# Optimization experiments

Measured on AMD Instinct MI355X. Metric: run time of the kernel, lower is better.

Reference implementation:

```python
import jax, jax.numpy as jnp
import numpy as np

E = 1024
H = 16
D = E // H  # head_dim = 64
B, L, S = 2, 2048, 2048


def setup_inputs() -> dict:
    key = jax.random.key(0)
    ks = jax.random.split(key, 10)
    scale = 1.0 / np.sqrt(E)
    return {
        "x": jax.random.normal(ks[0], (B, L, E), jnp.float32),
        "context": jax.random.normal(ks[1], (B, S, E), jnp.float32),
        "Wq": jax.random.normal(ks[2], (E, E), jnp.float32) * scale,
        "bq": jnp.zeros((E,), jnp.float32),
        "Wk": jax.random.normal(ks[3], (E, E), jnp.float32) * scale,
        "bk": jnp.zeros((E,), jnp.float32),
        "Wv": jax.random.normal(ks[4], (E, E), jnp.float32) * scale,
        "bv": jnp.zeros((E,), jnp.float32),
        "Wp": jax.random.normal(ks[5], (E, E), jnp.float32) * scale,
        "bp": jnp.zeros((E,), jnp.float32),
    }


def reference(x, context, Wq, bq, Wk, bk, Wv, bv, Wp, bp):
    b, l, _ = x.shape
    s = context.shape[1]
    # linear projections then split heads: [B, H, L/S, D]
    q = (x @ Wq + bq).reshape(b, l, H, D).transpose(0, 2, 1, 3)
    k = (context @ Wk + bk).reshape(b, s, H, D).transpose(0, 2, 1, 3)
    v = (context @ Wv + bv).reshape(b, s, H, D).transpose(0, 2, 1, 3)
    # scores [B, H, L, S]
    attn = jnp.einsum("bhld,bhsd->bhls", q, k) / jnp.sqrt(jnp.float32(D))
    attn = jax.nn.softmax(attn, axis=-1)
    # dropout is identity in eval mode
    out = jnp.einsum("bhls,bhsd->bhld", attn, v)
    out = out.transpose(0, 2, 1, 3).reshape(b, l, E)
    return out @ Wp + bp
```

## Files before the change

### kernel.cpp

```cpp
#include <hip/hip_runtime.h>
#include <math.h>

#define B_ 2
#define L_ 2048
#define S_ 2048
#define E_ 1024
#define H_ 16
#define D_ 64
#define SC_ 0.180336880111120f

typedef unsigned short u16;
typedef unsigned int u32;
typedef __attribute__((ext_vector_type(8))) short short8;
typedef __attribute__((ext_vector_type(4))) float floatx4;

__device__ __forceinline__ u16 f2bf(float f) {
    union { float f; unsigned u; } a; a.f = f;
    unsigned r = a.u + 0x7FFFu + ((a.u >> 16) & 1u);
    return (u16)(r >> 16);
}

__device__ __forceinline__ u32 cvt_pk_bf16(float lo, float hi) {
    u32 d;
    asm("v_cvt_pk_bf16_f32 %0, %1, %2" : "=v"(d) : "v"(lo), "v"(hi));
    return d;
}

__device__ __forceinline__ void pl32swap(u32& a, u32& b) {
    asm("v_permlane32_swap_b32 %0, %1" : "+v"(a), "+v"(b));
}
__device__ __forceinline__ void pl16swap(u32& a, u32& b) {
    asm("v_permlane16_swap_b32 %0, %1" : "+v"(a), "+v"(b));
}

__device__ __forceinline__ void glds16(const u16* g, u16* l) {
    __builtin_amdgcn_global_load_lds(
        (const __attribute__((address_space(1))) void*)g,
        (__attribute__((address_space(3))) void*)l, 16, 0, 0);
}

__global__ void prep_kernel(const float* __restrict__ x, const float* __restrict__ ctx,
                            u16* __restrict__ Xb, u16* __restrict__ Cb,
                            const float* __restrict__ Wq, const float* __restrict__ Wk,
                            const float* __restrict__ Wv, const float* __restrict__ Wp,
                            u16* __restrict__ WqT, u16* __restrict__ WkT,
                            u16* __restrict__ WvT, u16* __restrict__ WpT) {
    __shared__ float tile[32][33];
    const int bid = blockIdx.x;
    const int tid = threadIdx.x;
    if (bid < 4096) {
        const int sub = bid;
        const float* src = sub < 2048 ? x : ctx;
        u16* dst = sub < 2048 ? Xb : Cb;
        int i = (sub & 2047) * 256 + tid;
        float4 u0 = ((const float4*)src)[2 * i];
        float4 u1 = ((const float4*)src)[2 * i + 1];
        uint4 o;
        o.x = cvt_pk_bf16(u0.x, u0.y);
        o.y = cvt_pk_bf16(u0.z, u0.w);
        o.z = cvt_pk_bf16(u1.x, u1.y);
        o.w = cvt_pk_bf16(u1.z, u1.w);
        ((uint4*)dst)[i] = o;
    } else {
        const int t = bid - 4096;
        const int z = t >> 10;
        const int rem = t & 1023;
        const float* W = z == 0 ? Wq : (z == 1 ? Wk : (z == 2 ? Wv : Wp));
        u16* Wt = z == 0 ? WqT : (z == 1 ? WkT : (z == 2 ? WvT : WpT));
        const int bx = (rem & 31) * 32, by = (rem >> 5) * 32;
        const int tx = tid & 31, ty = tid >> 5;
#pragma unroll
        for (int j = 0; j < 4; ++j)
            tile[ty + j * 8][tx] = W[(size_t)(by + ty + j * 8) * E_ + bx + tx];
        __syncthreads();
#pragma unroll
        for (int j = 0; j < 4; ++j)
            Wt[(size_t)(bx + ty + j * 8) * E_ + by + tx] = f2bf(tile[tx][ty + j * 8]);
    }
}

__device__ __forceinline__ void xcd_remap64(int bx, int by, int& m_idx, int& n_idx) {
    int lin = bx + 8 * by;
    int c8 = lin & 7;
    int g = lin >> 3;
    m_idx = c8 + 8 * (g & 7);
    n_idx = g >> 3;
}

__global__ __launch_bounds__(256, 3) void qkv_gemm_kernel(
    const u16* __restrict__ Xb, const u16* __restrict__ Cb,
    const u16* __restrict__ WqT, const u16* __restrict__ WkT, const u16* __restrict__ WvT,
    const float* __restrict__ bq, const float* __restrict__ bk, const float* __restrict__ bv,
    u16* __restrict__ Qb, u16* __restrict__ Kb, u16* __restrict__ Vtb) {
    __shared__ __align__(16) u16 sm[24576];

    const int z = blockIdx.z;
    const u16* A  = z == 0 ? Xb : Cb;
    const u16* Bt = z == 0 ? WqT : (z == 1 ? WkT : WvT);
    const float* bias = z == 0 ? bq : (z == 1 ? bk : bv);
    const float scale = z == 0 ? SC_ : 1.0f;

    const int tid = threadIdx.x;
    const int lane = tid & 63;
    const int wv = tid >> 6;
    const int wm = wv >> 1, wn = wv & 1;
    const int qd = lane >> 4, lr = lane & 15;
    int m_idx, n_idx;
    xcd_remap64(blockIdx.x, blockIdx.y, m_idx, n_idx);
    const int m0 = m_idx * 64, n0 = n_idx * 128;
    const int lrow = lane >> 3;
    const int gu = (lane & 7) ^ lrow;

    floatx4 acc[2][4];
#pragma unroll
    for (int i = 0; i < 2; ++i)
#pragma unroll
        for (int j = 0; j < 4; ++j) {
            floatx4 zz = {0.f, 0.f, 0.f, 0.f};
            acc[i][j] = zz;
        }

#define STAGE_AB(buf, kb)                                                          \
    {                                                                              \
        _Pragma("unroll") for (int j = 0; j < 2; ++j) {                            \
            int c = wv * 2 + j;                                                    \
            glds16(A + (size_t)(m0 + c * 8 + lrow) * E_ + (kb) + gu * 8,           \
                   sm + (buf)*4096 + c * 512);                                     \
        }                                                                          \
        _Pragma("unroll") for (int j = 0; j < 4; ++j) {                            \
            int c = wv * 4 + j;                                                    \
            glds16(Bt + (size_t)(n0 + c * 8 + lrow) * E_ + (kb) + gu * 8,          \
                   sm + 8192 + (buf)*8192 + c * 512);                              \
        }                                                                          \
    }

    STAGE_AB(0, 0)
    __syncthreads();

    for (int t = 0; t < 16; ++t) {
        const int cur = t & 1;
        if (t + 1 < 16) STAGE_AB(cur ^ 1, (t + 1) * 64)

        short8 af[2][2], bf[4][2];
#pragma unroll
        for (int mi = 0; mi < 2; ++mi)
#pragma unroll
            for (int kk = 0; kk < 2; ++kk) {
                int row = wm * 32 + mi * 16 + lr;
                int u = (kk * 4 + qd) ^ (lr & 7);
                af[mi][kk] = *(const short8*)(sm + cur * 4096 + row * 64 + u * 8);
            }
#pragma unroll
        for (int ni = 0; ni < 4; ++ni)
#pragma unroll
            for (int kk = 0; kk < 2; ++kk) {
                int row = wn * 64 + ni * 16 + lr;
                int u = (kk * 4 + qd) ^ (lr & 7);
                bf[ni][kk] = *(const short8*)(sm + 8192 + cur * 8192 + row * 64 + u * 8);
            }
        __builtin_amdgcn_s_setprio(1);
#pragma unroll
        for (int kk = 0; kk < 2; ++kk)
#pragma unroll
            for (int mi = 0; mi < 2; ++mi)
#pragma unroll
                for (int ni = 0; ni < 4; ++ni)
                    acc[mi][ni] = __builtin_amdgcn_mfma_f32_16x16x32_bf16(
                        af[mi][kk], bf[ni][kk], acc[mi][ni], 0, 0, 0);
        __builtin_amdgcn_s_setprio(0);

        __syncthreads();
    }

    if (z == 2) {
        const int CTS = 72;
#pragma unroll
        for (int mi = 0; mi < 2; ++mi)
#pragma unroll
            for (int ni = 0; ni < 4; ++ni) {
                int col = wn * 64 + ni * 16 + lr;
                int row = wm * 32 + mi * 16 + qd * 4;
                float bv_ = bias[n0 + col];
                u16 h0 = f2bf(acc[mi][ni][0] + bv_);
                u16 h1 = f2bf(acc[mi][ni][1] + bv_);
                u16 h2 = f2bf(acc[mi][ni][2] + bv_);
                u16 h3 = f2bf(acc[mi][ni][3] + bv_);
                uint2 pk;
                pk.x = h0 | ((u32)h1 << 16);
                pk.y = h2 | ((u32)h3 << 16);
                *(uint2*)&sm[col * CTS + row] = pk;
            }
        __syncthreads();
        const int d = tid >> 1;
        const int sh = (tid & 1) * 32;
        const int bidx = m0 >> 11;
        const int sloc = m0 & (S_ - 1);
        u16* dstV = Vtb + ((size_t)(bidx * E_ + n0 + d)) * S_ + sloc + sh;
        const u16* srcC = sm + d * CTS + sh;
#pragma unroll
        for (int j = 0; j < 4; ++j)
            *(uint4*)(dstV + j * 8) = *(const uint4*)(srcC + j * 8);
    } else {
        u16* Cq = z == 0 ? Qb : Kb;
#pragma unroll
        for (int mi = 0; mi < 2; ++mi) {
#pragma unroll
            for (int ni = 0; ni < 4; ++ni) {
                int col = n0 + wn * 64 + ni * 16 + lr;
                float bv_ = bias[col];
#pragma unroll
                for (int r = 0; r < 4; ++r) {
                    int row = m0 + wm * 32 + mi * 16 + qd * 4 + r;
                    Cq[(size_t)row * E_ + col] = f2bf((acc[mi][ni][r] + bv_) * scale);
                }
            }
        }
    }
#undef STAGE_AB
}

__global__ __launch_bounds__(256, 4) void flash_attn_kernel(
    const u16* __restrict__ Q, const u16* __restrict__ Kg,
    const u16* __restrict__ Vtg, u16* __restrict__ Opart, float* __restrict__ lpart) {
    __shared__ __align__(16) u16 Ks[2][64 * 64];
    __shared__ __align__(16) u16 Vs[2][64 * 64];

    const int tid = threadIdx.x;
    const int lane = tid & 63;
    const int wv = tid >> 6;
    const int qd = lane >> 4, lr = lane & 15;

    const int lin = blockIdx.x + 16 * (blockIdx.y + 32 * blockIdx.z);
    const int c8 = lin & 7;
    const int slot = lin >> 3;
    const int qx = slot & 15;
    const int grp = c8 + 8 * (slot >> 4);
    const int bh = grp & 31;
    const int z = grp >> 5;
    const int b = bh >> 4, h = bh & 15;
    const int q0 = qx * 128;
    const int sbeg = z * (S_ / 2);

    u16* Op = Opart + (size_t)z * (B_ * L_ * E_);
    float* lp = lpart + (size_t)z * (B_ * H_ * L_);

    const u16* Kbase = Kg + (size_t)(b * S_) * E_ + h * D_;
    const u16* Vbase = Vtg + (size_t)(b * E_ + h * D_) * S_;

    const int lrow = lane >> 3;
    const int gu = (lane & 7) ^ lrow;

#pragma unroll
    for (int j = 0; j < 2; ++j) {
        int c = wv * 2 + j;
        glds16(Kbase + (size_t)(sbeg + c * 8 + lrow) * E_ + gu * 8, &Ks[0][c * 512]);
        glds16(Vbase + (size_t)(c * 8 + lrow) * S_ + sbeg + gu * 8, &Vs[0][c * 512]);
    }

    short8 qf[2][2];
#pragma unroll
    for (int mi = 0; mi < 2; ++mi)
#pragma unroll
        for (int kk = 0; kk < 2; ++kk)
            qf[mi][kk] = *(const short8*)(Q + (size_t)(b * L_ + q0 + wv * 32 + mi * 16 + lr) * E_ +
                                          h * D_ + kk * 32 + qd * 8);

    const short one_bf = (short)0x3F80;
    short8 ones8 = {one_bf, one_bf, one_bf, one_bf, one_bf, one_bf, one_bf, one_bf};

    floatx4 o_acc[2][4];
    floatx4 l4[2];
#pragma unroll
    for (int mi = 0; mi < 2; ++mi) {
#pragma unroll
        for (int nt = 0; nt < 4; ++nt) {
            floatx4 z4 = {0.f, 0.f, 0.f, 0.f};
            o_acc[mi][nt] = z4;
        }
        floatx4 z4 = {0.f, 0.f, 0.f, 0.f};
        l4[mi] = z4;
    }

    __syncthreads();

    const int NIT = (S_ / 2) / 64;

    for (int it = 0; it < NIT; ++it) {
        const int cur = it & 1;
        if (it + 1 < NIT) {
            int s1 = sbeg + (it + 1) * 64;
#pragma unroll
            for (int j = 0; j < 2; ++j) {
                int c = wv * 2 + j;
                glds16(Kbase + (size_t)(s1 + c * 8 + lrow) * E_ + gu * 8, &Ks[cur ^ 1][c * 512]);
                glds16(Vbase + (size_t)(c * 8 + lrow) * S_ + s1 + gu * 8, &Vs[cur ^ 1][c * 512]);
            }
        }

        floatx4 s_[2][4];
        __builtin_amdgcn_s_setprio(1);
#pragma unroll
        for (int nt = 0; nt < 4; ++nt) {
            int krow = nt * 16 + lr;
            short8 kb0 = *(const short8*)(&Ks[cur][krow * 64 + ((qd) ^ (lr & 7)) * 8]);
            short8 kb1 = *(const short8*)(&Ks[cur][krow * 64 + ((4 + qd) ^ (lr & 7)) * 8]);
#pragma unroll
            for (int mi = 0; mi < 2; ++mi) {
                floatx4 zz = {0.f, 0.f, 0.f, 0.f};
                zz = __builtin_amdgcn_mfma_f32_16x16x32_bf16(kb0, qf[mi][0], zz, 0, 0, 0);
                zz = __builtin_amdgcn_mfma_f32_16x16x32_bf16(kb1, qf[mi][1], zz, 0, 0, 0);
                s_[mi][nt] = zz;
            }
        }
        __builtin_amdgcn_s_setprio(0);

        short8 pf[2][2];
#pragma unroll
        for (int mi = 0; mi < 2; ++mi) {
            u32 dg[4][2];
#pragma unroll
            for (int nt = 0; nt < 4; ++nt) {
                float p0 = __builtin_amdgcn_exp2f(s_[mi][nt][0]);
                float p1 = __builtin_amdgcn_exp2f(s_[mi][nt][1]);
                float p2 = __builtin_amdgcn_exp2f(s_[mi][nt][2]);
                float p3 = __builtin_amdgcn_exp2f(s_[mi][nt][3]);
                dg[nt][0] = cvt_pk_bf16(p0, p1);
                dg[nt][1] = cvt_pk_bf16(p2, p3);
            }
#pragma unroll
            for (int kk = 0; kk < 2; ++kk) {
                u32 x0 = dg[2 * kk][0], y0 = dg[2 * kk + 1][0];
                pl32swap(x0, y0);
                pl16swap(x0, y0);
                u32 x1 = dg[2 * kk][1], y1 = dg[2 * kk + 1][1];
                pl32swap(x1, y1);
                pl16swap(x1, y1);
                union { u32 d[4]; short8 v; } u;
                u.d[0] = x0; u.d[1] = x1; u.d[2] = y0; u.d[3] = y1;
                pf[mi][kk] = u.v;
            }
        }

        __builtin_amdgcn_s_setprio(1);
#pragma unroll
        for (int mi = 0; mi < 2; ++mi) {
            l4[mi] = __builtin_amdgcn_mfma_f32_16x16x32_bf16(pf[mi][0], ones8, l4[mi], 0, 0, 0);
            l4[mi] = __builtin_amdgcn_mfma_f32_16x16x32_bf16(pf[mi][1], ones8, l4[mi], 0, 0, 0);
        }
#pragma unroll
        for (int nt = 0; nt < 4; ++nt) {
            int vrow = nt * 16 + lr;
            short8 vb0 = *(const short8*)(&Vs[cur][vrow * 64 + ((qd) ^ (lr & 7)) * 8]);
            short8 vb1 = *(const short8*)(&Vs[cur][vrow * 64 + ((4 + qd) ^ (lr & 7)) * 8]);
#pragma unroll
            for (int mi = 0; mi < 2; ++mi) {
                o_acc[mi][nt] = __builtin_amdgcn_mfma_f32_16x16x32_bf16(pf[mi][0], vb0, o_acc[mi][nt], 0, 0, 0);
                o_acc[mi][nt] = __builtin_amdgcn_mfma_f32_16x16x32_bf16(pf[mi][1], vb1, o_acc[mi][nt], 0, 0, 0);
            }
        }
        __builtin_amdgcn_s_setprio(0);

        __syncthreads();
    }

    float linv[2][4];
#pragma unroll
    for (int mi = 0; mi < 2; ++mi) {
        if (lr == 0) {
#pragma unroll
            for (int r = 0; r < 4; ++r)
                lp[(size_t)(b * H_ + h) * L_ + q0 + wv * 32 + mi * 16 + qd * 4 + r] = l4[mi][r];
        }
#pragma unroll
        for (int r = 0; r < 4; ++r) linv[mi][r] = 1.0f / l4[mi][r];
    }

#pragma unroll
    for (int mi = 0; mi < 2; ++mi)
#pragma unroll
        for (int nt = 0; nt < 4; ++nt)
#pragma unroll
            for (int r = 0; r < 4; ++r) {
                int row = q0 + wv * 32 + mi * 16 + qd * 4 + r;
                int col = h * D_ + nt * 16 + lr;
                Op[(size_t)(b * L_ + row) * E_ + col] = f2bf(o_acc[mi][nt][r] * linv[mi][r]);
            }
}

__global__ __launch_bounds__(256, 2) void out_gemm_kernel(
    const u16* __restrict__ O1, const u16* __restrict__ O2,
    const float* __restrict__ l1, const float* __restrict__ l2,
    const u16* __restrict__ WpT, const float* __restrict__ bp,
    float* __restrict__ out) {
    __shared__ __align__(16) u16 As[2][64 * 64];
    __shared__ __align__(16) u16 Bs[2][128 * 64];

    const int tid = threadIdx.x;
    const int lane = tid & 63;
    const int wv = tid >> 6;
    const int wm = wv >> 1, wn = wv & 1;
    const int qd = lane >> 4, lr = lane & 15;

    int m_idx, n_idx;
    xcd_remap64(blockIdx.x, blockIdx.y, m_idx, n_idx);
    const int m0 = m_idx * 64, n0 = n_idx * 128;
    const int lrow = lane >> 3;
    const int gu = (lane & 7) ^ lrow;

    floatx4 acc[2][4];
#pragma unroll
    for (int i = 0; i < 2; ++i)
#pragma unroll
        for (int j = 0; j < 4; ++j) {
            floatx4 zz = {0.f, 0.f, 0.f, 0.f};
            acc[i][j] = zz;
        }

    uint4 p1[2], p2[2];
    float la_[2], lb_[2];

#define LOAD_AO(tt)                                                                \
    {                                                                              \
        _Pragma("unroll") for (int j = 0; j < 2; ++j) {                            \
            int c = wv * 2 + j;                                                    \
            int row = m0 + c * 8 + lrow;                                           \
            int col = (tt)*64 + gu * 8;                                            \
            p1[j] = *(const uint4*)(O1 + (size_t)row * E_ + col);                  \
            p2[j] = *(const uint4*)(O2 + (size_t)row * E_ + col);                  \
            int li = (row >> 11) * (H_ * L_) + (tt)*L_ + (row & (L_ - 1));         \
            la_[j] = l1[li];                                                       \
            lb_[j] = l2[li];                                                       \
        }                                                                          \
    }

#define WRITE_AO(buf)                                                              \
    {                                                                              \
        _Pragma("unroll") for (int j = 0; j < 2; ++j) {                            \
            int c = wv * 2 + j;                                                    \
            float s = 1.0f / (la_[j] + lb_[j]);                                    \
            float w1 = la_[j] * s, w2 = lb_[j] * s;                                \
            const u32* pa = (const u32*)&p1[j];                                    \
            const u32* pb = (const u32*)&p2[j];                                    \
            uint4 o;                                                               \
            u32* po = (u32*)&o;                                                    \
            _Pragma("unroll") for (int d = 0; d < 4; ++d) {                        \
                union { u32 u; float f; } x0, x1, y0, y1;                          \
                x0.u = pa[d] << 16; x1.u = pa[d] & 0xFFFF0000u;                    \
                y0.u = pb[d] << 16; y1.u = pb[d] & 0xFFFF0000u;                    \
                po[d] = cvt_pk_bf16(x0.f * w1 + y0.f * w2, x1.f * w1 + y1.f * w2); \
            }                                                                      \
            *(uint4*)(&As[buf][c * 512 + lane * 8]) = o;                           \
        }                                                                          \
    }

#define STAGE_BO(buf, kb)                                                          \
    {                                                                              \
        _Pragma("unroll") for (int j = 0; j < 4; ++j) {                            \
            int c = wv * 4 + j;                                                    \
            glds16(WpT + (size_t)(n0 + c * 8 + lrow) * E_ + (kb) + gu * 8,         \
                   &Bs[buf][c * 512]);                                             \
        }                                                                          \
    }

    LOAD_AO(0)
    STAGE_BO(0, 0)
    WRITE_AO(0)
    __syncthreads();

    for (int t = 0; t < 16; ++t) {
        const int cur = t & 1;
        if (t + 1 < 16) {
            STAGE_BO(cur ^ 1, (t + 1) * 64)
            LOAD_AO(t + 1)
        }

        short8 af[2][2], bf[4][2];
#pragma unroll
        for (int mi = 0; mi < 2; ++mi)
#pragma unroll
            for (int kk = 0; kk < 2; ++kk) {
                int row = wm * 32 + mi * 16 + lr;
                int u = (kk * 4 + qd) ^ (lr & 7);
                af[mi][kk] = *(const short8*)(&As[cur][row * 64 + u * 8]);
            }
#pragma unroll
        for (int ni = 0; ni < 4; ++ni)
#pragma unroll
            for (int kk = 0; kk < 2; ++kk) {
                int row = wn * 64 + ni * 16 + lr;
                int u = (kk * 4 + qd) ^ (lr & 7);
                bf[ni][kk] = *(const short8*)(&Bs[cur][row * 64 + u * 8]);
            }
        __builtin_amdgcn_s_setprio(1);
#pragma unroll
        for (int kk = 0; kk < 2; ++kk)
#pragma unroll
            for (int mi = 0; mi < 2; ++mi)
#pragma unroll
                for (int ni = 0; ni < 4; ++ni)
                    acc[mi][ni] = __builtin_amdgcn_mfma_f32_16x16x32_bf16(
                        af[mi][kk], bf[ni][kk], acc[mi][ni], 0, 0, 0);
        __builtin_amdgcn_s_setprio(0);

        if (t + 1 < 16) WRITE_AO(cur ^ 1)
        __syncthreads();
    }

#pragma unroll
    for (int mi = 0; mi < 2; ++mi)
#pragma unroll
        for (int ni = 0; ni < 4; ++ni) {
            int col = n0 + wn * 64 + ni * 16 + lr;
            float bv_ = bp[col];
#pragma unroll
            for (int r = 0; r < 4; ++r) {
                int row = m0 + wm * 32 + mi * 16 + qd * 4 + r;
                out[(size_t)row * E_ + col] = acc[mi][ni][r] + bv_;
            }
        }
#undef LOAD_AO
#undef WRITE_AO
#undef STAGE_BO
}

extern "C" void kernel_launch(void* const* d_in, const int* in_sizes, int n_in,
                              void* d_out, int out_size, void* d_ws, size_t ws_size,
                              hipStream_t stream) {
    const float* x   = (const float*)d_in[0];
    const float* ctx = (const float*)d_in[1];
    const float* Wq  = (const float*)d_in[2];
    const float* bq  = (const float*)d_in[3];
    const float* Wk  = (const float*)d_in[4];
    const float* bk  = (const float*)d_in[5];
    const float* Wv  = (const float*)d_in[6];
    const float* bv  = (const float*)d_in[7];
    const float* Wp  = (const float*)d_in[8];
    const float* bp  = (const float*)d_in[9];
    float* out = (float*)d_out;

    u16* WqT = (u16*)d_ws;
    u16* WkT = WqT + 1048576;
    u16* WvT = WkT + 1048576;
    u16* WpT = WvT + 1048576;
    u16* Qb  = WpT + 1048576;
    u16* Kb  = Qb + 4194304;
    u16* Vtb = Kb + 4194304;
    u16* Xb  = Vtb + 4194304;
    u16* Cb  = Xb + 4194304;
    u16* Opart = Xb;
    float* lpart = (float*)(Cb + 4194304);
    (void)ws_size; (void)in_sizes; (void)n_in; (void)out_size;

    prep_kernel<<<dim3(8192), 256, 0, stream>>>(
        x, ctx, Xb, Cb, Wq, Wk, Wv, Wp, WqT, WkT, WvT, WpT);

    qkv_gemm_kernel<<<dim3(8, 64, 3), 256, 0, stream>>>(
        Xb, Cb, WqT, WkT, WvT, bq, bk, bv, Qb, Kb, Vtb);

    flash_attn_kernel<<<dim3(L_ / 128, B_ * H_, 2), 256, 0, stream>>>(
        Qb, Kb, Vtb, Opart, lpart);

    out_gemm_kernel<<<dim3(8, 64), 256, 0, stream>>>(
        Opart, Opart + 4194304, lpart, lpart + B_ * H_ * L_, WpT, bp, out);
}
```

Baseline: 198.3 us.

## Fuse K and V projections into one block sharing the context tile

The QKV GEMM grid drops from three z-slices to two: z=0 computes Q, and z=1 computes both K and V from a single staged context tile, with an extra LDS buffer for the Wv tile and a second accumulator set. This halves the loads of the shared A operand for K/V and removes one launch slice. In exchange, the z=1 blocks do twice the work, which creates load imbalance between z=0 and z=1. Register and LDS use also grow, so launch bounds drop from 3 to 2 blocks per CU, lowering occupancy.

Result: no change. 198.8 us (+0.3%).

```diff
diff --git a/kernel.cpp b/kernel.cpp
--- a/kernel.cpp
+++ b/kernel.cpp
@@ -87,18 +87,16 @@
     n_idx = g >> 3;
 }
 
-__global__ __launch_bounds__(256, 3) void qkv_gemm_kernel(
+__global__ __launch_bounds__(256, 2) void qkv_gemm_kernel(
     const u16* __restrict__ Xb, const u16* __restrict__ Cb,
     const u16* __restrict__ WqT, const u16* __restrict__ WkT, const u16* __restrict__ WvT,
     const float* __restrict__ bq, const float* __restrict__ bk, const float* __restrict__ bv,
     u16* __restrict__ Qb, u16* __restrict__ Kb, u16* __restrict__ Vtb) {
-    __shared__ __align__(16) u16 sm[24576];
+    __shared__ __align__(16) u16 sm[40960];
 
     const int z = blockIdx.z;
-    const u16* A  = z == 0 ? Xb : Cb;
-    const u16* Bt = z == 0 ? WqT : (z == 1 ? WkT : WvT);
-    const float* bias = z == 0 ? bq : (z == 1 ? bk : bv);
-    const float scale = z == 0 ? SC_ : 1.0f;
+    const u16* A   = z == 0 ? Xb : Cb;
+    const u16* Btk = z == 0 ? WqT : WkT;
 
     const int tid = threadIdx.x;
     const int lane = tid & 63;
@@ -111,13 +109,14 @@
     const int lrow = lane >> 3;
     const int gu = (lane & 7) ^ lrow;
 
-    floatx4 acc[2][4];
+    floatx4 acck[2][4], accv[2][4];
 #pragma unroll
     for (int i = 0; i < 2; ++i)
 #pragma unroll
         for (int j = 0; j < 4; ++j) {
             floatx4 zz = {0.f, 0.f, 0.f, 0.f};
-            acc[i][j] = zz;
+            acck[i][j] = zz;
+            accv[i][j] = zz;
         }
 
 #define STAGE_AB(buf, kb)                                                          \
@@ -129,8 +128,15 @@
         }                                                                          \
         _Pragma("unroll") for (int j = 0; j < 4; ++j) {                            \
             int c = wv * 4 + j;                                                    \
-            glds16(Bt + (size_t)(n0 + c * 8 + lrow) * E_ + (kb) + gu * 8,          \
+            glds16(Btk + (size_t)(n0 + c * 8 + lrow) * E_ + (kb) + gu * 8,         \
                    sm + 8192 + (buf)*8192 + c * 512);                              \
+        }                                                                          \
+        if (z == 1) {                                                              \
+            _Pragma("unroll") for (int j = 0; j < 4; ++j) {                        \
+                int c = wv * 4 + j;                                                \
+                glds16(WvT + (size_t)(n0 + c * 8 + lrow) * E_ + (kb) + gu * 8,     \
+                       sm + 24576 + (buf)*8192 + c * 512);                         \
+            }                                                                      \
         }                                                                          \
     }
 
@@ -141,7 +147,7 @@
         const int cur = t & 1;
         if (t + 1 < 16) STAGE_AB(cur ^ 1, (t + 1) * 64)
 
-        short8 af[2][2], bf[4][2];
+        short8 af[2][2];
 #pragma unroll
         for (int mi = 0; mi < 2; ++mi)
 #pragma unroll
@@ -150,29 +156,78 @@
                 int u = (kk * 4 + qd) ^ (lr & 7);
                 af[mi][kk] = *(const short8*)(sm + cur * 4096 + row * 64 + u * 8);
             }
-#pragma unroll
-        for (int ni = 0; ni < 4; ++ni)
-#pragma unroll
-            for (int kk = 0; kk < 2; ++kk) {
-                int row = wn * 64 + ni * 16 + lr;
-                int u = (kk * 4 + qd) ^ (lr & 7);
-                bf[ni][kk] = *(const short8*)(sm + 8192 + cur * 8192 + row * 64 + u * 8);
-            }
-        __builtin_amdgcn_s_setprio(1);
-#pragma unroll
-        for (int kk = 0; kk < 2; ++kk)
-#pragma unroll
-            for (int mi = 0; mi < 2; ++mi)
-#pragma unroll
-                for (int ni = 0; ni < 4; ++ni)
-                    acc[mi][ni] = __builtin_amdgcn_mfma_f32_16x16x32_bf16(
-                        af[mi][kk], bf[ni][kk], acc[mi][ni], 0, 0, 0);
-        __builtin_amdgcn_s_setprio(0);
+        {
+            short8 bfk[4][2];
+#pragma unroll
+            for (int ni = 0; ni < 4; ++ni)
+#pragma unroll
+                for (int kk = 0; kk < 2; ++kk) {
+                    int row = wn * 64 + ni * 16 + lr;
+                    int u = (kk * 4 + qd) ^ (lr & 7);
+                    bfk[ni][kk] = *(const short8*)(sm + 8192 + cur * 8192 + row * 64 + u * 8);
+                }
+            __builtin_amdgcn_s_setprio(1);
+#pragma unroll
+            for (int kk = 0; kk < 2; ++kk)
+#pragma unroll
+                for (int mi = 0; mi < 2; ++mi)
+#pragma unroll
+                    for (int ni = 0; ni < 4; ++ni)
+                        acck[mi][ni] = __builtin_amdgcn_mfma_f32_16x16x32_bf16(
+                            af[mi][kk], bfk[ni][kk], acck[mi][ni], 0, 0, 0);
+            __builtin_amdgcn_s_setprio(0);
+        }
+        if (z == 1) {
+            short8 bfv[4][2];
+#pragma unroll
+            for (int ni = 0; ni < 4; ++ni)
+#pragma unroll
+                for (int kk = 0; kk < 2; ++kk) {
+                    int row = wn * 64 + ni * 16 + lr;
+                    int u = (kk * 4 + qd) ^ (lr & 7);
+                    bfv[ni][kk] = *(const short8*)(sm + 24576 + cur * 8192 + row * 64 + u * 8);
+                }
+            __builtin_amdgcn_s_setprio(1);
+#pragma unroll
+            for (int kk = 0; kk < 2; ++kk)
+#pragma unroll
+                for (int mi = 0; mi < 2; ++mi)
+#pragma unroll
+                    for (int ni = 0; ni < 4; ++ni)
+                        accv[mi][ni] = __builtin_amdgcn_mfma_f32_16x16x32_bf16(
+                            af[mi][kk], bfv[ni][kk], accv[mi][ni], 0, 0, 0);
+            __builtin_amdgcn_s_setprio(0);
+        }
 
         __syncthreads();
     }
 
-    if (z == 2) {
+    if (z == 0) {
+#pragma unroll
+        for (int mi = 0; mi < 2; ++mi)
+#pragma unroll
+            for (int ni = 0; ni < 4; ++ni) {
+                int col = n0 + wn * 64 + ni * 16 + lr;
+                float bv_ = bq[col];
+#pragma unroll
+                for (int r = 0; r < 4; ++r) {
+                    int row = m0 + wm * 32 + mi * 16 + qd * 4 + r;
+                    Qb[(size_t)row * E_ + col] = f2bf((acck[mi][ni][r] + bv_) * SC_);
+                }
+            }
+    } else {
+#pragma unroll
+        for (int mi = 0; mi < 2; ++mi)
+#pragma unroll
+            for (int ni = 0; ni < 4; ++ni) {
+                int col = n0 + wn * 64 + ni * 16 + lr;
+                float bv_ = bk[col];
+#pragma unroll
+                for (int r = 0; r < 4; ++r) {
+                    int row = m0 + wm * 32 + mi * 16 + qd * 4 + r;
+                    Kb[(size_t)row * E_ + col] = f2bf(acck[mi][ni][r] + bv_);
+                }
+            }
         const int CTS = 72;
 #pragma unroll
         for (int mi = 0; mi < 2; ++mi)
@@ -180,11 +235,11 @@
             for (int ni = 0; ni < 4; ++ni) {
                 int col = wn * 64 + ni * 16 + lr;
                 int row = wm * 32 + mi * 16 + qd * 4;
-                float bv_ = bias[n0 + col];
-                u16 h0 = f2bf(acc[mi][ni][0] + bv_);
-                u16 h1 = f2bf(acc[mi][ni][1] + bv_);
-                u16 h2 = f2bf(acc[mi][ni][2] + bv_);
-                u16 h3 = f2bf(acc[mi][ni][3] + bv_);
+                float bv_ = bv[n0 + col];
+                u16 h0 = f2bf(accv[mi][ni][0] + bv_);
+                u16 h1 = f2bf(accv[mi][ni][1] + bv_);
+                u16 h2 = f2bf(accv[mi][ni][2] + bv_);
+                u16 h3 = f2bf(accv[mi][ni][3] + bv_);
                 uint2 pk;
                 pk.x = h0 | ((u32)h1 << 16);
                 pk.y = h2 | ((u32)h3 << 16);
@@ -200,21 +255,6 @@
 #pragma unroll
         for (int j = 0; j < 4; ++j)
             *(uint4*)(dstV + j * 8) = *(const uint4*)(srcC + j * 8);
-    } else {
-        u16* Cq = z == 0 ? Qb : Kb;
-#pragma unroll
-        for (int mi = 0; mi < 2; ++mi) {
-#pragma unroll
-            for (int ni = 0; ni < 4; ++ni) {
-                int col = n0 + wn * 64 + ni * 16 + lr;
-                float bv_ = bias[col];
-#pragma unroll
-                for (int r = 0; r < 4; ++r) {
-                    int row = m0 + wm * 32 + mi * 16 + qd * 4 + r;
-                    Cq[(size_t)row * E_ + col] = f2bf((acc[mi][ni][r] + bv_) * scale);
-                }
-            }
-        }
     }
 #undef STAGE_AB
 }
@@ -554,7 +594,7 @@
     prep_kernel<<<dim3(8192), 256, 0, stream>>>(
         x, ctx, Xb, Cb, Wq, Wk, Wv, Wp, WqT, WkT, WvT, WpT);
 
-    qkv_gemm_kernel<<<dim3(8, 64, 3), 256, 0, stream>>>(
+    qkv_gemm_kernel<<<dim3(8, 64, 2), 256, 0, stream>>>(
         Xb, Cb, WqT, WkT, WvT, bq, bk, bv, Qb, Kb, Vtb);
 
     flash_attn_kernel<<<dim3(L_ / 128, B_ * H_, 2), 256, 0, stream>>>(
```
